# Performance work log

Hardware: AMD Instinct MI355X
Metric: run time of the kernel (lower is better)

The kernel has to match this reference:

```python
import jax, jax.numpy as jnp
import numpy as np

B, N, Q, Z, C, L = 1, 6, 20000, 4, 128, 4
IMG_H, IMG_W = 256, 704
PC_RANGE = (-50.0, -50.0, -4.0, 50.0, 50.0, 4.0)
NUM_FREQS = 10
EPS = 1e-5
LEVEL_HW = ((64, 176), (32, 88), (16, 44), (8, 22))


def _mlp(x, ws, bs):
    for i, (w, b) in enumerate(zip(ws, bs)):
        x = x @ w + b
        if i < len(ws) - 1:
            x = jax.nn.relu(x)
    return x


def _bilinear(feat_hwc, px, py):
    # feat_hwc: [H, W, C]; px, py: [P] pixel coords. align_corners=False, zero padding.
    H, W, _ = feat_hwc.shape
    x0 = jnp.floor(px).astype(jnp.int32)
    y0 = jnp.floor(py).astype(jnp.int32)
    wx = px - x0
    wy = py - y0

    def gather(yi, xi):
        inb = ((yi >= 0) & (yi < H) & (xi >= 0) & (xi < W)).astype(feat_hwc.dtype)
        return feat_hwc[jnp.clip(yi, 0, H - 1), jnp.clip(xi, 0, W - 1)] * inb[:, None]

    return (gather(y0, x0) * ((1 - wy) * (1 - wx))[:, None]
          + gather(y0, x0 + 1) * ((1 - wy) * wx)[:, None]
          + gather(y0 + 1, x0) * (wy * (1 - wx))[:, None]
          + gather(y0 + 1, x0 + 1) * (wy * wx)[:, None])


def _pointbev_forward(feats, reference_points, lidar2img,
                      pe_w1, pe_b1, pe_w2, pe_b2, wt_w, wt_b, hm_ws, hm_bs):
    pos = jnp.transpose(reference_points, (0, 2, 1, 3))            # [B,Q,Z,3] in [0,1]
    # sinusoidal positional encoding map (normalized=False: coords used as-is)
    freqs = (2.0 ** jnp.arange(NUM_FREQS, dtype=pos.dtype)) * jnp.pi
    ang = pos[..., None] * freqs                                   # [B,Q,Z,3,F]
    pe_in = jnp.concatenate([jnp.sin(ang), jnp.cos(ang)], axis=-1)
    pe_in = pe_in.reshape(pos.shape[:-1] + (3 * 2 * NUM_FREQS,))
    pos_emb = _mlp(pe_in, [pe_w1, pe_w2], [pe_b1, pe_b2])          # [B,Q,Z,C]
    scale_w = jax.nn.softmax(pos_emb @ wt_w + wt_b, axis=-1)       # [B,Q,Z,L]

    # unnormalize to metric lidar coords via pc_range
    lo = jnp.asarray(PC_RANGE[:3], pos.dtype)
    span = jnp.asarray(PC_RANGE[3:], pos.dtype) - lo
    pts4 = jnp.concatenate([pos * span + lo, jnp.ones_like(pos[..., :1])], axis=-1)
    cam = jnp.einsum('bnij,bqzj->bnqzi', lidar2img, pts4)          # [B,N,Q,Z,4]
    homo = cam[..., 2]
    uv = cam[..., :2] / jnp.maximum(homo, EPS)[..., None]
    u = uv[..., 0] / IMG_W
    v = uv[..., 1] / IMG_H
    valid = ((homo > EPS) & (u > 0.0) & (u < 1.0) & (v > 0.0) & (v < 1.0)).astype(pos.dtype)

    sampler = jax.vmap(_bilinear)
    uf = u.reshape(B * N, Q * Z)
    vf = v.reshape(B * N, Q * Z)
    out = jnp.zeros((B, Q, Z, C), pos.dtype)
    for l, feat in enumerate(feats):                               # L=4 fixed levels
        Hl, Wl = feat.shape[2], feat.shape[3]
        s = sampler(feat.reshape(B * N, Hl, Wl, C), uf * Wl - 0.5, vf * Hl - 0.5)
        s = s.reshape(B, N, Q, Z, C) * valid[..., None]            # mask invalid projections
        out = out + s.sum(axis=1) * scale_w[..., l, None]          # sum views, weight level
    out = (out + pos_emb).reshape(B, Q, Z * C)
    return _mlp(out, hm_ws, hm_bs)                                 # [B,Q,C]


def setup_inputs():
    key = jax.random.key(0)
    ks = jax.random.split(key, 32)
    inp = {}
    for l, (h, w) in enumerate(LEVEL_HW):
        inp[f"feat{l}"] = jax.random.normal(ks[l], (B, N, h, w, C), jnp.float32)
    inp["reference_points"] = jax.random.uniform(ks[8], (B, Z, Q, 3), jnp.float32)
    # structured nuScenes-like lidar2img = intrinsics @ extrinsics for a 6-camera ring
    l2i = np.zeros((B, N, 4, 4), np.float32)
    K = np.array([[400.0, 0.0, IMG_W / 2, 0.0],
                  [0.0, 400.0, IMG_H / 2, 0.0],
                  [0.0, 0.0, 1.0, 0.0],
                  [0.0, 0.0, 0.0, 1.0]], np.float32)
    for n in range(N):
        yaw = 2.0 * np.pi * n / N
        cy, sy = np.cos(yaw), np.sin(yaw)
        R = np.array([[-sy, cy, 0.0], [0.0, 0.0, -1.0], [cy, sy, 0.0]], np.float32)
        E = np.eye(4, dtype=np.float32)
        E[:3, :3] = R
        E[:3, 3] = [0.0, 1.5, 0.5]
        l2i[0, n] = K @ E
    inp["lidar2img"] = jnp.asarray(l2i)

    def lin(k, fi, fo):
        s = 1.0 / np.sqrt(fi)
        return jax.random.uniform(k, (fi, fo), jnp.float32, -s, s)

    d_in = 3 * 2 * NUM_FREQS
    inp["pe_w1"] = lin(ks[9], d_in, 2 * C); inp["pe_b1"] = jnp.zeros((2 * C,), jnp.float32)
    inp["pe_w2"] = lin(ks[10], 2 * C, C);   inp["pe_b2"] = jnp.zeros((C,), jnp.float32)
    inp["wt_w"] = lin(ks[11], C, L);        inp["wt_b"] = jnp.zeros((L,), jnp.float32)
    dims = [Z * C, 2 * Z * C, 2 * Z * C, 2 * Z * C, C]
    for i in range(4):
        inp[f"hm_w{i+1}"] = lin(ks[12 + i], dims[i], dims[i + 1])
        inp[f"hm_b{i+1}"] = jnp.zeros((dims[i + 1],), jnp.float32)
    return inp


def reference(feat0, feat1, feat2, feat3, reference_points, lidar2img,
              pe_w1, pe_b1, pe_w2, pe_b2, wt_w, wt_b,
              hm_w1, hm_b1, hm_w2, hm_b2, hm_w3, hm_b3, hm_w4, hm_b4):
    return _pointbev_forward((feat0, feat1, feat2, feat3), reference_points, lidar2img,
                             pe_w1, pe_b1, pe_w2, pe_b2, wt_w, wt_b,
                             [hm_w1, hm_w2, hm_w3, hm_w4], [hm_b1, hm_b2, hm_b3, hm_b4])
```

## Files before the change

### kernel.cpp

```cpp
#include <hip/hip_runtime.h>
#include <math.h>

#define QN 20000
#define PN 80000
#define CN 128
#define NVIEW 6

typedef __attribute__((ext_vector_type(8))) _Float16 h8;
typedef __attribute__((ext_vector_type(4))) _Float16 h4;
typedef __attribute__((ext_vector_type(4))) float f32x4;

__device__ __forceinline__ void gload16(const void* g, void* l) {
  __builtin_amdgcn_global_load_lds(
      (const __attribute__((address_space(1))) void*)g,
      (__attribute__((address_space(3))) void*)l, 16, 0, 0);
}

__global__ __launch_bounds__(256) void wtrans_all(
    const float* __restrict__ w0, const float* __restrict__ w1,
    const float* __restrict__ w2, const float* __restrict__ w3,
    const float* __restrict__ w4, const float* __restrict__ w5,
    _Float16* __restrict__ base) {
  __shared__ float t[32][33];
  int b = blockIdx.x;
  const float* W; _Float16* T; int K, N, Kp, nbx, lb;
  if (b < 16)        { W = w0; T = base + 0;       K = 60;   N = 256;  Kp = 64;   nbx = 8;  lb = b; }
  else if (b < 48)   { W = w1; T = base + 32768;   K = 256;  N = 128;  Kp = 256;  nbx = 4;  lb = b - 16; }
  else if (b < 560)  { W = w2; T = base + 98304;   K = 512;  N = 1024; Kp = 512;  nbx = 32; lb = b - 48; }
  else if (b < 1584) { W = w3; T = base + 1146880; K = 1024; N = 1024; Kp = 1024; nbx = 32; lb = b - 560; }
  else if (b < 2608) { W = w4; T = base + 3244032; K = 1024; N = 1024; Kp = 1024; nbx = 32; lb = b - 1584; }
  else               { W = w5; T = base + 5341184; K = 1024; N = 128;  Kp = 1024; nbx = 4;  lb = b - 2608; }
  const int n0 = (lb % nbx) * 32, k0 = (lb / nbx) * 32;
  const int tx = threadIdx.x & 31, ty = threadIdx.x >> 5;
  #pragma unroll
  for (int j = 0; j < 4; ++j) {
    int k = k0 + ty + j * 8;
    t[ty + j * 8][tx] = (k < K) ? W[(size_t)k * N + n0 + tx] : 0.f;
  }
  __syncthreads();
  #pragma unroll
  for (int j = 0; j < 4; ++j) {
    int n = n0 + ty + j * 8;
    int k = k0 + tx;
    T[(size_t)n * Kp + k] = (_Float16)t[tx][ty + j * 8];
  }
}

__global__ __launch_bounds__(256) void fcvt_kernel(
    const float* __restrict__ s0, const float* __restrict__ s1,
    const float* __restrict__ s2, const float* __restrict__ s3,
    _Float16* __restrict__ d) {
  size_t i = (size_t)blockIdx.x * 256 + threadIdx.x;
  if (i >= 2872320) return;
  const float* s; size_t off;
  if (i < 2162688)      { s = s0; off = 0; }
  else if (i < 2703360) { s = s1; off = 2162688; }
  else if (i < 2838528) { s = s2; off = 2703360; }
  else                  { s = s3; off = 2838528; }
  f32x4 v = *(const f32x4*)(s + (i - off) * 4);
  h4 o;
  o[0] = (_Float16)v[0]; o[1] = (_Float16)v[1];
  o[2] = (_Float16)v[2]; o[3] = (_Float16)v[3];
  *(h4*)(d + i * 4) = o;
}

__global__ __launch_bounds__(256) void pe_in_kernel(const float* __restrict__ rp,
                                                    _Float16* __restrict__ P) {
  int idx = blockIdx.x * 256 + threadIdx.x;
  if (idx >= PN * 64) return;
  int p = idx >> 6, k = idx & 63;
  float val = 0.f;
  if (k < 60) {
    int q = p >> 2, z = p & 3;
    int d = k / 20, r = k - d * 20;
    int j = (r >= 10) ? (r - 10) : r;
    float pos = rp[((size_t)z * QN + q) * 3 + d];
    float ang = pos * ((float)(1 << j) * 3.14159265358979323846f);
    val = (r >= 10) ? cosf(ang) : sinf(ang);
  }
  P[idx] = (_Float16)val;
}

__global__ __launch_bounds__(256) void lw_kernel(const _Float16* __restrict__ posE,
                                                 const float* __restrict__ wtw,
                                                 const float* __restrict__ wtb,
                                                 float* __restrict__ lw) {
  __shared__ float swtT[512];
  __shared__ float sb[4];
  const int tid = threadIdx.x;
  for (int i = tid; i < 512; i += 256) swtT[(i & 3) * 128 + (i >> 2)] = wtw[i];
  if (tid < 4) sb[tid] = wtb[tid];
  __syncthreads();

  const int wave = tid >> 6, lane = tid & 63;
  const int grp = lane >> 4, s = lane & 15;
  const int p = blockIdx.x * 16 + wave * 4 + grp;
  const int c0 = s * 8;
  h8 pa = *(const h8*)(posE + (size_t)p * CN + c0);

  float lg[4];
  #pragma unroll
  for (int l = 0; l < 4; ++l) {
    const float* w = swtT + l * 128 + c0;
    float acc = 0.f;
    #pragma unroll
    for (int j = 0; j < 8; ++j) acc = fmaf((float)pa[j], w[j], acc);
    lg[l] = acc;
  }
  #pragma unroll
  for (int off = 8; off > 0; off >>= 1) {
    lg[0] += __shfl_xor(lg[0], off);
    lg[1] += __shfl_xor(lg[1], off);
    lg[2] += __shfl_xor(lg[2], off);
    lg[3] += __shfl_xor(lg[3], off);
  }
  lg[0] += sb[0]; lg[1] += sb[1]; lg[2] += sb[2]; lg[3] += sb[3];
  float mx = fmaxf(fmaxf(lg[0], lg[1]), fmaxf(lg[2], lg[3]));
  float e0 = __expf(lg[0] - mx), e1 = __expf(lg[1] - mx);
  float e2 = __expf(lg[2] - mx), e3 = __expf(lg[3] - mx);
  float esr = 1.f / (e0 + e1 + e2 + e3);
  if (s == 0) {
    f32x4 o = {e0 * esr, e1 * esr, e2 * esr, e3 * esr};
    *(f32x4*)(lw + (size_t)p * 4) = o;
  }
}

template <bool RELU, int OUT>
__global__ __launch_bounds__(256, 4) void gemm_h(const _Float16* __restrict__ A,
                                                 const _Float16* __restrict__ B,
                                                 const float* __restrict__ bias,
                                                 float* __restrict__ Cf,
                                                 _Float16* __restrict__ Ch,
                                                 int M, int N, int K,
                                                 int nbn) {
  __shared__ _Float16 sm[2][2][4096];
  const int tid = threadIdx.x;
  const int wave = tid >> 6, lane = tid & 63;
  const int wr = wave >> 1, wc = wave & 1;
  const int g = lane >> 4, r16 = lane & 15;

  const int nwg = gridDim.x;
  const int q8 = nwg >> 3, r8 = nwg & 7;
  const int xcd = blockIdx.x & 7, sub = blockIdx.x >> 3;
  const int wg = (xcd < r8 ? xcd * (q8 + 1) : r8 * (q8 + 1) + (xcd - r8) * q8) + sub;
  const int bn = (wg % nbn) * 128;
  const int bm = (wg / nbn) * 128;
  const int nt = K >> 5;

  f32x4 acc[4][4];
  #pragma unroll
  for (int i = 0; i < 4; ++i)
    #pragma unroll
    for (int j = 0; j < 4; ++j) acc[i][j] = {0.f, 0.f, 0.f, 0.f};

  auto STAGE = [&](int buf, int t) {
    const int kof = t << 5;
    const int rsub = lane >> 2;
    const int slot0 = lane & 3;
    #pragma unroll
    for (int pl = 0; pl < 2; ++pl) {
      const _Float16* P = (pl == 0) ? A : B;
      const int rbase = (pl == 0) ? bm : bn;
      #pragma unroll
      for (int i = 0; i < 2; ++i) {
        int group = wave * 2 + i;
        int row = group * 16 + rsub;
        int slot = slot0 ^ ((row >> 1) & 3);
        int gr = rbase + row;
        if (pl == 0 && gr >= M) gr = M - 1;
        gload16(P + (size_t)gr * K + kof + slot * 8,
                &sm[buf][pl][group * 512]);
      }
    }
  };

  auto COMPUTE = [&](int buf) {
    h8 a[4], b[4];
    #pragma unroll
    for (int mi = 0; mi < 4; ++mi) {
      int row = wr * 64 + mi * 16 + r16;
      int off = row * 32 + ((g ^ ((row >> 1) & 3)) * 8);
      a[mi] = *(const h8*)&sm[buf][0][off];
    }
    #pragma unroll
    for (int ni = 0; ni < 4; ++ni) {
      int row = wc * 64 + ni * 16 + r16;
      int off = row * 32 + ((g ^ ((row >> 1) & 3)) * 8);
      b[ni] = *(const h8*)&sm[buf][1][off];
    }
    #pragma unroll
    for (int mi = 0; mi < 4; ++mi)
      #pragma unroll
      for (int ni = 0; ni < 4; ++ni)
        acc[mi][ni] = __builtin_amdgcn_mfma_f32_16x16x32_f16(a[mi], b[ni], acc[mi][ni], 0, 0, 0);
  };

  STAGE(0, 0);
  __syncthreads();

  for (int t = 0; t < nt; ++t) {
    if (t + 1 < nt) STAGE((t + 1) & 1, t + 1);
    COMPUTE(t & 1);
    __syncthreads();
  }

  #pragma unroll
  for (int mi = 0; mi < 4; ++mi) {
    int gr0 = bm + wr * 64 + mi * 16 + (lane >> 4) * 4;
    #pragma unroll
    for (int ni = 0; ni < 4; ++ni) {
      int gc = bn + wc * 64 + ni * 16 + r16;
      float bv = bias[gc];
      #pragma unroll
      for (int r = 0; r < 4; ++r) {
        int row = gr0 + r;
        if (row >= M) continue;
        float v = acc[mi][ni][r] + bv;
        if (RELU) v = fmaxf(v, 0.f);
        if (OUT == 0) Cf[(size_t)row * N + gc] = v;
        else          Ch[(size_t)row * N + gc] = (_Float16)v;
      }
    }
  }
}

template <bool RELU, int OUT>
__global__ __launch_bounds__(128, 3) void gemm_h64(const _Float16* __restrict__ A,
                                                   const _Float16* __restrict__ B,
                                                   const float* __restrict__ bias,
                                                   float* __restrict__ Cf,
                                                   _Float16* __restrict__ Ch,
                                                   int M, int N, int K,
                                                   int nbn) {
  __shared__ _Float16 smA[2][64 * 32];
  __shared__ _Float16 smB[2][128 * 32];
  const int tid = threadIdx.x;
  const int wave = tid >> 6, lane = tid & 63;
  const int wc = wave;
  const int g = lane >> 4, r16 = lane & 15;

  const int nwg = gridDim.x;
  const int q8 = nwg >> 3, r8 = nwg & 7;
  const int xcd = blockIdx.x & 7, sub = blockIdx.x >> 3;
  const int wg = (xcd < r8 ? xcd * (q8 + 1) : r8 * (q8 + 1) + (xcd - r8) * q8) + sub;
  const int bn = (wg % nbn) * 128;
  const int bm = (wg / nbn) * 64;
  const int nt = K >> 5;

  f32x4 acc[4][4];
  #pragma unroll
  for (int i = 0; i < 4; ++i)
    #pragma unroll
    for (int j = 0; j < 4; ++j) acc[i][j] = {0.f, 0.f, 0.f, 0.f};

  auto STAGE = [&](int buf, int t) {
    const int kof = t << 5;
    const int rsub = lane >> 2;
    const int slot0 = lane & 3;
    #pragma unroll
    for (int i = 0; i < 2; ++i) {
      int group = wave * 2 + i;
      int row = group * 16 + rsub;
      int slot = slot0 ^ ((row >> 1) & 3);
      int gr = bm + row; if (gr >= M) gr = M - 1;
      gload16(A + (size_t)gr * K + kof + slot * 8, &smA[buf][group * 512]);
    }
    #pragma unroll
    for (int i = 0; i < 4; ++i) {
      int group = wave * 4 + i;
      int row = group * 16 + rsub;
      int slot = slot0 ^ ((row >> 1) & 3);
      gload16(B + (size_t)(bn + row) * K + kof + slot * 8, &smB[buf][group * 512]);
    }
  };

  auto COMPUTE = [&](int buf) {
    h8 a[4], b[4];
    #pragma unroll
    for (int mi = 0; mi < 4; ++mi) {
      int row = mi * 16 + r16;
      int off = row * 32 + ((g ^ ((row >> 1) & 3)) * 8);
      a[mi] = *(const h8*)&smA[buf][off];
    }
    #pragma unroll
    for (int ni = 0; ni < 4; ++ni) {
      int row = wc * 64 + ni * 16 + r16;
      int off = row * 32 + ((g ^ ((row >> 1) & 3)) * 8);
      b[ni] = *(const h8*)&smB[buf][off];
    }
    #pragma unroll
    for (int mi = 0; mi < 4; ++mi)
      #pragma unroll
      for (int ni = 0; ni < 4; ++ni)
        acc[mi][ni] = __builtin_amdgcn_mfma_f32_16x16x32_f16(a[mi], b[ni], acc[mi][ni], 0, 0, 0);
  };

  STAGE(0, 0);
  __syncthreads();

  for (int t = 0; t < nt; ++t) {
    if (t + 1 < nt) STAGE((t + 1) & 1, t + 1);
    COMPUTE(t & 1);
    __syncthreads();
  }

  #pragma unroll
  for (int mi = 0; mi < 4; ++mi) {
    int gr0 = bm + mi * 16 + (lane >> 4) * 4;
    #pragma unroll
    for (int ni = 0; ni < 4; ++ni) {
      int gc = bn + wc * 64 + ni * 16 + r16;
      float bv = bias[gc];
      #pragma unroll
      for (int r = 0; r < 4; ++r) {
        int row = gr0 + r;
        if (row >= M) continue;
        float v = acc[mi][ni][r] + bv;
        if (RELU) v = fmaxf(v, 0.f);
        if (OUT == 0) Cf[(size_t)row * N + gc] = v;
        else          Ch[(size_t)row * N + gc] = (_Float16)v;
      }
    }
  }
}

__global__ __launch_bounds__(256) void sample_kernel(
    const _Float16* __restrict__ fbase,
    const float* __restrict__ rp, const float* __restrict__ l2i,
    const float* __restrict__ lw,
    const _Float16* __restrict__ posE, _Float16* __restrict__ X0) {
  __shared__ float sl2i[96];
  const int tid = threadIdx.x;
  if (tid < 96) sl2i[tid] = l2i[tid];
  __syncthreads();

  const _Float16* FL[4] = {fbase, fbase + 8650752, fbase + 10813440,
                           fbase + 11354112};

  const int wave = tid >> 6, lane = tid & 63;
  const int half = lane >> 5, s = lane & 31;
  const int p = blockIdx.x * 8 + wave * 2 + half;
  const int q = p >> 2, z = p & 3;

  const float X  = rp[((size_t)z * QN + q) * 3 + 0] * 100.f - 50.f;
  const float Y  = rp[((size_t)z * QN + q) * 3 + 1] * 100.f - 50.f;
  const float Zc = rp[((size_t)z * QN + q) * 3 + 2] * 8.f - 4.f;

  const int c0 = s * 4;
  h4 pa = *(const h4*)(posE + (size_t)p * CN + c0);
  const float pe0 = (float)pa[0], pe1 = (float)pa[1];
  const float pe2 = (float)pa[2], pe3 = (float)pa[3];

  f32x4 lw4 = *(const f32x4*)(lw + (size_t)p * 4);
  float swl[4] = {lw4[0], lw4[1], lw4[2], lw4[3]};

  float a0 = 0.f, a1 = 0.f, a2 = 0.f, a3 = 0.f;
  for (int n = 0; n < NVIEW; n++) {
    const float* Mx = sl2i + n * 16;
    float cam0 = Mx[0] * X + Mx[1] * Y + Mx[2]  * Zc + Mx[3];
    float cam1 = Mx[4] * X + Mx[5] * Y + Mx[6]  * Zc + Mx[7];
    float cam2 = Mx[8] * X + Mx[9] * Y + Mx[10] * Zc + Mx[11];
    float denom = fmaxf(cam2, 1e-5f);
    float u = cam0 / denom * (1.f / 704.f);
    float v = cam1 / denom * (1.f / 256.f);
    bool valid = (cam2 > 1e-5f) & (u > 0.f) & (u < 1.f) & (v > 0.f) & (v < 1.f);
    if (!valid) continue;
    float px3 = u * 22.f - 0.5f, py3 = v * 8.f - 0.5f;
    bool interior = (px3 >= 0.f) & (py3 >= 0.f) & (px3 < 21.f) & (py3 < 7.f);
    if (interior) {
      #pragma unroll
      for (int l = 0; l < 4; l++) {
        const int Hl = 64 >> l, Wl = 176 >> l;
        float pxl = u * (float)Wl - 0.5f;
        float pyl = v * (float)Hl - 0.5f;
        float fx = floorf(pxl), fy = floorf(pyl);
        int x0 = (int)fx, y0 = (int)fy;
        float wx = pxl - fx, wy = pyl - fy;
        float w1r = wy * swl[l], w0r = swl[l] - w1r;
        float w01 = w0r * wx, w00 = w0r - w01;
        float w11 = w1r * wx, w10 = w1r - w11;
        const _Float16* cp = FL[l]
            + ((size_t)n * (Hl * Wl) + (size_t)(y0 * Wl + x0)) * CN + c0;
        h4 v00 = *(const h4*)(cp);
        h4 v01 = *(const h4*)(cp + CN);
        h4 v10 = *(const h4*)(cp + Wl * CN);
        h4 v11 = *(const h4*)(cp + Wl * CN + CN);
        a0 = fmaf(w00, (float)v00[0], fmaf(w01, (float)v01[0], fmaf(w10, (float)v10[0], fmaf(w11, (float)v11[0], a0))));
        a1 = fmaf(w00, (float)v00[1], fmaf(w01, (float)v01[1], fmaf(w10, (float)v10[1], fmaf(w11, (float)v11[1], a1))));
        a2 = fmaf(w00, (float)v00[2], fmaf(w01, (float)v01[2], fmaf(w10, (float)v10[2], fmaf(w11, (float)v11[2], a2))));
        a3 = fmaf(w00, (float)v00[3], fmaf(w01, (float)v01[3], fmaf(w10, (float)v10[3], fmaf(w11, (float)v11[3], a3))));
      }
    } else {
      #pragma unroll
      for (int l = 0; l < 4; l++) {
        const int Hl = 64 >> l, Wl = 176 >> l;
        float pxl = u * (float)Wl - 0.5f;
        float pyl = v * (float)Hl - 0.5f;
        float fx = floorf(pxl), fy = floorf(pyl);
        int x0 = (int)fx, y0 = (int)fy;
        float wx = pxl - fx, wy = pyl - fy;
        float w1r = wy * swl[l], w0r = swl[l] - w1r;
        const float wxs[2] = {1.f - wx, wx};
        const float wrs[2] = {w0r, w1r};
        const _Float16* fb = FL[l] + (size_t)n * (Hl * Wl) * CN;
        #pragma unroll
        for (int cy = 0; cy < 2; cy++) {
          #pragma unroll
          for (int cx = 0; cx < 2; cx++) {
            int xi = x0 + cx, yi = y0 + cy;
            bool inb = ((unsigned)xi < (unsigned)Wl) & ((unsigned)yi < (unsigned)Hl);
            int off = inb ? (yi * Wl + xi) * CN : 0;
            float wgt = inb ? (wrs[cy] * wxs[cx]) : 0.f;
            h4 vv = *(const h4*)(fb + off + c0);
            a0 = fmaf(wgt, (float)vv[0], a0);
            a1 = fmaf(wgt, (float)vv[1], a1);
            a2 = fmaf(wgt, (float)vv[2], a2);
            a3 = fmaf(wgt, (float)vv[3], a3);
          }
        }
      }
    }
  }
  h4 o;
  o[0] = (_Float16)(a0 + pe0);
  o[1] = (_Float16)(a1 + pe1);
  o[2] = (_Float16)(a2 + pe2);
  o[3] = (_Float16)(a3 + pe3);
  *(h4*)&X0[(size_t)p * CN + c0] = o;
}

extern "C" void kernel_launch(void* const* d_in, const int* in_sizes, int n_in,
                              void* d_out, int out_size, void* d_ws, size_t ws_size,
                              hipStream_t stream) {
  const float* feat0 = (const float*)d_in[0];
  const float* feat1 = (const float*)d_in[1];
  const float* feat2 = (const float*)d_in[2];
  const float* feat3 = (const float*)d_in[3];
  const float* rp    = (const float*)d_in[4];
  const float* l2i   = (const float*)d_in[5];
  const float* pe_w1 = (const float*)d_in[6];
  const float* pe_b1 = (const float*)d_in[7];
  const float* pe_w2 = (const float*)d_in[8];
  const float* pe_b2 = (const float*)d_in[9];
  const float* wt_w  = (const float*)d_in[10];
  const float* wt_b  = (const float*)d_in[11];
  const float* hm_w1 = (const float*)d_in[12];
  const float* hm_b1 = (const float*)d_in[13];
  const float* hm_w2 = (const float*)d_in[14];
  const float* hm_b2 = (const float*)d_in[15];
  const float* hm_w3 = (const float*)d_in[16];
  const float* hm_b3 = (const float*)d_in[17];
  const float* hm_w4 = (const float*)d_in[18];
  const float* hm_b4 = (const float*)d_in[19];
  float* out = (float*)d_out;

  char* ws = (char*)d_ws;
  typedef _Float16 h16;
  h16* wPE1 = (h16*)(ws + 0);
  h16* wPE2 = (h16*)(ws + 65536);
  h16* wH1  = (h16*)(ws + 196608);
  h16* wH2  = (h16*)(ws + 2293760);
  h16* wH3  = (h16*)(ws + 6488064);
  h16* wH4  = (h16*)(ws + 10682368);

  h16*   posE = (h16*)(ws + 11534336);
  float* lwga = (float*)(ws + 33000000);
  h16*   hpe  = (h16*)(ws + 53000192);
  h16*   pein = (h16*)(ws + 94000128);
  h16*   X0   = (h16*)(ws + 53000192);
  h16*   H1   = (h16*)(ws + 94000128);
  h16*   H2   = (h16*)(ws + 11534336);
  h16*   H3   = (h16*)(ws + 94000128);
  h16*   f16b = (h16*)(ws + 136000000);

  wtrans_all<<<2736, 256, 0, stream>>>(pe_w1, pe_w2, hm_w1, hm_w2, hm_w3, hm_w4,
                                       (h16*)ws);
  fcvt_kernel<<<(2872320 + 255) / 256, 256, 0, stream>>>(feat0, feat1, feat2,
                                                         feat3, f16b);

  pe_in_kernel<<<(PN * 64 + 255) / 256, 256, 0, stream>>>(rp, pein);

  gemm_h<true, 1><<<2 * 625, 256, 0, stream>>>(pein, wPE1, pe_b1, nullptr, hpe, PN, 256, 64, 2);
  gemm_h64<false, 1><<<1250, 128, 0, stream>>>(hpe, wPE2, pe_b2, nullptr, posE, PN, 128, 256, 1);

  lw_kernel<<<PN / 16, 256, 0, stream>>>(posE, wt_w, wt_b, lwga);

  sample_kernel<<<PN / 8, 256, 0, stream>>>(f16b, rp, l2i, lwga, posE, X0);

  gemm_h<true, 1><<<8 * 157, 256, 0, stream>>>(X0, wH1, hm_b1, nullptr, H1, QN, 1024, 512, 8);
  gemm_h<true, 1><<<8 * 157, 256, 0, stream>>>(H1, wH2, hm_b2, nullptr, H2, QN, 1024, 1024, 8);
  gemm_h<true, 1><<<8 * 157, 256, 0, stream>>>(H2, wH3, hm_b3, nullptr, H3, QN, 1024, 1024, 8);
  gemm_h64<false, 0><<<313, 128, 0, stream>>>(H3, wH4, hm_b4, out, nullptr, QN, 128, 1024, 1);
}
```

Before: 322.6 us.

## Load GEMM B operand directly into registers, stage only A in LDS

The GEMM kernel stops staging the weight (B) tile through LDS and instead has each wave load its B fragments straight from global memory into registers, double-buffered in registers across iterations. Only A goes through LDS now, which halves LDS traffic and footprint. The main loop is unrolled by two with ping-pong buffers. It assumes nt is even, raises register pressure (launch bounds drop from 4 to 3 blocks), and B rows are loaded redundantly by waves sharing wc, relying on the cache.

```diff
diff --git a/kernel.cpp b/kernel.cpp
--- a/kernel.cpp
+++ b/kernel.cpp
@@ -126,14 +126,14 @@
 }
 
 template <bool RELU, int OUT>
-__global__ __launch_bounds__(256, 4) void gemm_h(const _Float16* __restrict__ A,
+__global__ __launch_bounds__(256, 3) void gemm_h(const _Float16* __restrict__ A,
                                                  const _Float16* __restrict__ B,
                                                  const float* __restrict__ bias,
                                                  float* __restrict__ Cf,
                                                  _Float16* __restrict__ Ch,
                                                  int M, int N, int K,
                                                  int nbn) {
-  __shared__ _Float16 sm[2][2][4096];
+  __shared__ _Float16 smA[2][128 * 32];
   const int tid = threadIdx.x;
   const int wave = tid >> 6, lane = tid & 63;
   const int wr = wave >> 1, wc = wave & 1;
@@ -153,40 +153,37 @@
     #pragma unroll
     for (int j = 0; j < 4; ++j) acc[i][j] = {0.f, 0.f, 0.f, 0.f};
 
-  auto STAGE = [&](int buf, int t) {
+  auto STAGE_A = [&](int buf, int t) {
     const int kof = t << 5;
     const int rsub = lane >> 2;
     const int slot0 = lane & 3;
     #pragma unroll
-    for (int pl = 0; pl < 2; ++pl) {
-      const _Float16* P = (pl == 0) ? A : B;
-      const int rbase = (pl == 0) ? bm : bn;
-      #pragma unroll
-      for (int i = 0; i < 2; ++i) {
-        int group = wave * 2 + i;
-        int row = group * 16 + rsub;
-        int slot = slot0 ^ ((row >> 1) & 3);
-        int gr = rbase + row;
-        if (pl == 0 && gr >= M) gr = M - 1;
-        gload16(P + (size_t)gr * K + kof + slot * 8,
-                &sm[buf][pl][group * 512]);
-      }
+    for (int i = 0; i < 2; ++i) {
+      int group = wave * 2 + i;
+      int row = group * 16 + rsub;
+      int slot = slot0 ^ ((row >> 1) & 3);
+      int gr = bm + row; if (gr >= M) gr = M - 1;
+      gload16(A + (size_t)gr * K + kof + slot * 8,
+              &smA[buf][group * 512]);
     }
   };
 
-  auto COMPUTE = [&](int buf) {
-    h8 a[4], b[4];
+  auto B_LOAD = [&](h8* b, int t) {
+    const int kof = t << 5;
+    #pragma unroll
+    for (int ni = 0; ni < 4; ++ni) {
+      int row = bn + wc * 64 + ni * 16 + r16;
+      b[ni] = *(const h8*)(B + (size_t)row * K + kof + g * 8);
+    }
+  };
+
+  auto COMPUTE = [&](int buf, const h8* b) {
+    h8 a[4];
     #pragma unroll
     for (int mi = 0; mi < 4; ++mi) {
       int row = wr * 64 + mi * 16 + r16;
       int off = row * 32 + ((g ^ ((row >> 1) & 3)) * 8);
-      a[mi] = *(const h8*)&sm[buf][0][off];
-    }
-    #pragma unroll
-    for (int ni = 0; ni < 4; ++ni) {
-      int row = wc * 64 + ni * 16 + r16;
-      int off = row * 32 + ((g ^ ((row >> 1) & 3)) * 8);
-      b[ni] = *(const h8*)&sm[buf][1][off];
+      a[mi] = *(const h8*)&smA[buf][off];
     }
     #pragma unroll
     for (int mi = 0; mi < 4; ++mi)
@@ -195,12 +192,21 @@
         acc[mi][ni] = __builtin_amdgcn_mfma_f32_16x16x32_f16(a[mi], b[ni], acc[mi][ni], 0, 0, 0);
   };
 
-  STAGE(0, 0);
+  h8 b0[4], b1[4];
+  STAGE_A(0, 0);
+  B_LOAD(b0, 0);
   __syncthreads();
 
-  for (int t = 0; t < nt; ++t) {
-    if (t + 1 < nt) STAGE((t + 1) & 1, t + 1);
-    COMPUTE(t & 1);
+  for (int t = 0; t < nt; t += 2) {
+    STAGE_A(1, t + 1);
+    B_LOAD(b1, t + 1);
+    COMPUTE(0, b0);
+    __syncthreads();
+    if (t + 2 < nt) {
+      STAGE_A(0, t + 2);
+      B_LOAD(b0, t + 2);
+    }
+    COMPUTE(1, b1);
     __syncthreads();
   }
 
```

Result: slower. 421.3 us (+30.6%).
